# Optimization experiments

Measured on AMD Instinct MI355X. Metric: run time of the kernel, lower is better.

The kernel has to match this reference:

```python
import jax, jax.numpy as jnp
import numpy as np

B, T, C, H = 1, 4096, 3072, 24
D = C // H  # 128


def _make_rope_freqs(t, d):
    # comfy-style rotation matrices: [t, d//2, 2, 2] with rows [[cos,-sin],[sin,cos]]
    half = d // 2
    inv = 1.0 / (10000.0 ** (np.arange(half, dtype=np.float64) / half))
    ang = np.arange(t, dtype=np.float64)[:, None] * inv[None, :]
    cos, sin = np.cos(ang), np.sin(ang)
    f = np.stack([np.stack([cos, -sin], -1), np.stack([sin, cos], -1)], -2)
    return jnp.asarray(f, jnp.float32)


def setup_inputs() -> dict:
    key = jax.random.key(0)
    ks = jax.random.split(key, 6)
    s = 0.02  # typical init scale
    x = jax.random.normal(ks[0], (B, T, C), jnp.float32)
    context = jax.random.normal(ks[1], (B, T, C), jnp.float32)
    Wq = jax.random.normal(ks[2], (C, C), jnp.float32) * s
    Wk = jax.random.normal(ks[3], (C, C), jnp.float32) * s
    Wv = jax.random.normal(ks[4], (C, C), jnp.float32) * s
    Wo = jax.random.normal(ks[5], (C, C), jnp.float32) * s
    freqs = _make_rope_freqs(T, D)  # [T, D//2, 2, 2]
    return {"x": x, "context": context, "freqs": freqs,
            "Wq": Wq, "Wk": Wk, "Wv": Wv, "Wo": Wo}


def _apply_rope(t, freqs):
    # t: [B, T, H, D]; freqs: [T, D//2, 2, 2]
    b, tt, h, d = t.shape
    tr = t.reshape(b, tt, h, d // 2, 1, 2)
    f = freqs[:, None]  # [T, 1, D//2, 2, 2] -> broadcast over B, H
    out = f[..., 0] * tr[..., 0] + f[..., 1] * tr[..., 1]  # [B,T,H,D//2,2]
    return out.reshape(b, tt, h, d)


def reference(x, context, freqs, Wq, Wk, Wv, Wo):
    # QKV projections (torch Linear: y = x @ W.T), kept in BTHD layout
    q = (x @ Wq.T).reshape(B, T, H, D)
    k = (context @ Wk.T).reshape(B, -1, H, D)
    v = (context @ Wv.T).reshape(B, -1, H, D)
    # RoPE on q and k
    q = _apply_rope(q, freqs)
    k = _apply_rope(k, freqs)
    # SDPA, non-causal, scale 1/sqrt(D) (jax expects BTNH layout)
    out = jax.nn.dot_product_attention(q, k, v)
    return out.reshape(B, T, C) @ Wo.T
```

## Files before the change

### kernel.cpp

```cpp
#include <hip/hip_runtime.h>
#include <hip/hip_bf16.h>

#define TT 4096
#define CC 3072
#define HH 24
#define DD 128

typedef __bf16 bf16;
typedef __attribute__((ext_vector_type(8))) __bf16 bf16x8;
typedef __attribute__((ext_vector_type(4))) __bf16 bf16x4;
typedef __attribute__((ext_vector_type(4))) float f32x4;
typedef __attribute__((ext_vector_type(16))) float f32x16;
typedef __attribute__((ext_vector_type(4))) unsigned uint32x4;

#define MFMA(a,b,c)   __builtin_amdgcn_mfma_f32_16x16x32_bf16((a),(b),(c),0,0,0)
#define MFMA32(a,b,c) __builtin_amdgcn_mfma_f32_32x32x16_bf16((a),(b),(c),0,0,0)

static __device__ __forceinline__ unsigned packbf(float a, float b) {
  unsigned short ua = __builtin_bit_cast(unsigned short, (__bf16)a);
  unsigned short ub = __builtin_bit_cast(unsigned short, (__bf16)b);
  return (unsigned)ua | ((unsigned)ub << 16);
}
static __device__ __forceinline__ void plswap(unsigned &x, unsigned &y) {
  asm volatile("v_permlane32_swap_b32 %0, %1" : "+v"(x), "+v"(y));
}

template<int ABF, int OBF>
__global__ __launch_bounds__(256, 2)
void gemm_nt(const void* __restrict__ Ap, const float* __restrict__ Bp,
             void* __restrict__ Cp, int M, int N, int K) {
  __shared__ bf16 As[2][128][40];
  __shared__ bf16 Bs[2][128][40];
  const int tid = threadIdx.x;
  const int lane = tid & 63, wid = tid >> 6;
  const int m0 = blockIdx.y * 128, n0 = blockIdx.x * 128;
  const int wr = (wid >> 1) * 64, wc = (wid & 1) * 64;
  const int r = lane & 15, g = lane >> 4;
  const float* Af = (const float*)Ap;
  const bf16*  Ab = (const bf16*)Ap;

  f32x4 acc[4][4] = {};
  f32x4 pa[4], pb[4];
  bf16x8 qa[2];

  const int NT = K >> 5;

  auto load_tiles = [&](int kt) {
    const int kk = kt * 32;
    if constexpr (ABF) {
      #pragma unroll
      for (int j = 0; j < 2; ++j) {
        int c = tid + 256*j, row = c >> 2, kc = c & 3;
        qa[j] = *(const bf16x8*)(Ab + (size_t)(m0+row)*K + kk + kc*8);
      }
    } else {
      #pragma unroll
      for (int j = 0; j < 4; ++j) {
        int c = tid + 256*j, row = c >> 3, kc = c & 7;
        pa[j] = *(const f32x4*)(Af + (size_t)(m0+row)*K + kk + kc*4);
      }
    }
    #pragma unroll
    for (int j = 0; j < 4; ++j) {
      int c = tid + 256*j, row = c >> 3, kc = c & 7;
      pb[j] = *(const f32x4*)(Bp + (size_t)(n0+row)*K + kk + kc*4);
    }
  };

  auto write_tiles = [&](int buf) {
    if constexpr (ABF) {
      #pragma unroll
      for (int j = 0; j < 2; ++j) {
        int c = tid + 256*j, row = c >> 2, kc = c & 3;
        *(bf16x8*)&As[buf][row][kc*8] = qa[j];
      }
    } else {
      #pragma unroll
      for (int j = 0; j < 4; ++j) {
        int c = tid + 256*j, row = c >> 3, kc = c & 7;
        bf16x4 b;
        b[0]=(bf16)pa[j][0]; b[1]=(bf16)pa[j][1]; b[2]=(bf16)pa[j][2]; b[3]=(bf16)pa[j][3];
        *(bf16x4*)&As[buf][row][kc*4] = b;
      }
    }
    #pragma unroll
    for (int j = 0; j < 4; ++j) {
      int c = tid + 256*j, row = c >> 3, kc = c & 7;
      bf16x4 b;
      b[0]=(bf16)pb[j][0]; b[1]=(bf16)pb[j][1]; b[2]=(bf16)pb[j][2]; b[3]=(bf16)pb[j][3];
      *(bf16x4*)&Bs[buf][row][kc*4] = b;
    }
  };

  load_tiles(0);
  write_tiles(0);
  __syncthreads();

  for (int kt = 0; kt < NT; ++kt) {
    const int cur = kt & 1;
    if (kt + 1 < NT) load_tiles(kt + 1);
    bf16x8 af[4], bfr[4];
    #pragma unroll
    for (int m = 0; m < 4; ++m) af[m]  = *(const bf16x8*)&As[cur][wr + m*16 + r][g*8];
    #pragma unroll
    for (int n = 0; n < 4; ++n) bfr[n] = *(const bf16x8*)&Bs[cur][wc + n*16 + r][g*8];
    #pragma unroll
    for (int m = 0; m < 4; ++m)
      #pragma unroll
      for (int n = 0; n < 4; ++n)
        acc[m][n] = MFMA(af[m], bfr[n], acc[m][n]);
    if (kt + 1 < NT) write_tiles((kt + 1) & 1);
    __syncthreads();
  }

  #pragma unroll
  for (int m = 0; m < 4; ++m)
    #pragma unroll
    for (int n = 0; n < 4; ++n) {
      const int col = n0 + wc + n*16 + r;
      #pragma unroll
      for (int j = 0; j < 4; ++j) {
        const int row = m0 + wr + m*16 + g*4 + j;
        float v = acc[m][n][j];
        if constexpr (OBF) ((bf16*)Cp)[(size_t)row*N + col] = (bf16)v;
        else               ((float*)Cp)[(size_t)row*N + col] = v;
      }
    }
}

__global__ __launch_bounds__(256)
void rope_kernel(bf16* __restrict__ X, const float* __restrict__ F, float scale) {
  const int i = blockIdx.x * 256 + threadIdx.x;
  const size_t e8 = (size_t)i * 8;
  const int t  = (int)(e8 / CC);
  const int c  = (int)(e8 % CC);
  const int hc = c & (DD - 1);
  const float4* f = (const float4*)(F + (size_t)t*256 + (hc>>1)*4);
  bf16x8 v = *(const bf16x8*)(X + e8);
  bf16x8 o;
  #pragma unroll
  for (int p = 0; p < 4; ++p) {
    float x0 = (float)v[2*p], x1 = (float)v[2*p+1];
    float4 ff = f[p];
    o[2*p]   = (bf16)((ff.x*x0 + ff.y*x1) * scale);
    o[2*p+1] = (bf16)((ff.z*x0 + ff.w*x1) * scale);
  }
  *(bf16x8*)(X + e8) = o;
}

__global__ __launch_bounds__(256)
void transpose_v(const bf16* __restrict__ V, bf16* __restrict__ Vt) {
  __shared__ bf16 tile[64 * 128];
  const int t0 = blockIdx.x * 64, h = blockIdx.y;
  const int tid = threadIdx.x;
  #pragma unroll
  for (int j = 0; j < 4; ++j) {
    int c = tid + 256*j, t = c >> 4, c16 = c & 15;
    uint4 val = *(const uint4*)(V + (size_t)(t0+t)*CC + h*DD + c16*8);
    int sw = ((t & 7) ^ ((t >> 3) & 7)) << 4;
    *(uint4*)((char*)tile + t*256 + ((c16*16) ^ sw)) = val;
  }
  __syncthreads();
  #pragma unroll
  for (int j = 0; j < 4; ++j) {
    int c = tid + 256*j, d = c >> 3, c8 = c & 7;
    bf16x8 o;
    #pragma unroll
    for (int i = 0; i < 8; ++i) {
      int t = c8*8 + i;
      int sw = ((t & 7) ^ ((t >> 3) & 7)) << 4;
      o[i] = *(const bf16*)((char*)tile + t*256 + ((d*2) ^ sw));
    }
    *(bf16x8*)(Vt + (size_t)(h*DD + d)*TT + t0 + c8*8) = o;
  }
}

__global__ __launch_bounds__(256, 3)
void attn_kernel(const bf16* __restrict__ Q, const bf16* __restrict__ Kb,
                 const bf16* __restrict__ Vt, bf16* __restrict__ O) {
  __shared__ bf16 Ks[64 * 128];
  __shared__ bf16 Vs[128 * 64];

  const int tid = threadIdx.x, lane = tid & 63, wid = tid >> 6;
  const int c31 = lane & 31, g2 = lane >> 5;

  const int bid = blockIdx.x;
  const int fid = (bid & 7) * 96 + (bid >> 3);
  const int h = fid >> 5, qt = fid & 31;
  const int qrow = qt * 128 + wid * 32 + c31;

  bf16x8 aq[8];
  {
    const bf16* qp = Q + (size_t)qrow * CC + h * DD + g2 * 8;
    #pragma unroll
    for (int d0 = 0; d0 < 8; ++d0) aq[d0] = *(const bf16x8*)(qp + d0 * 16);
  }

  float m_ = -1e30f, l_ = 0.f;
  f32x16 o_[4] = {};

  auto stage = [&](int kv0) {
    uint4 kr[4], vr4[4];
    #pragma unroll
    for (int j = 0; j < 4; ++j) {
      int cc = tid + 256*j, row = cc >> 4, c16 = cc & 15;
      kr[j] = *(const uint4*)(Kb + (size_t)(kv0 + row) * CC + h * DD + c16 * 8);
    }
    #pragma unroll
    for (int j = 0; j < 4; ++j) {
      int cc = tid + 256*j, row = cc >> 3, c8 = cc & 7;
      vr4[j] = *(const uint4*)(Vt + (size_t)(h * DD + row) * TT + kv0 + c8 * 8);
    }
    #pragma unroll
    for (int j = 0; j < 4; ++j) {
      int cc = tid + 256*j, row = cc >> 4, c16 = cc & 15;
      *(uint4*)((char*)Ks + row * 256 + ((c16 * 16) ^ ((row & 7) << 4))) = kr[j];
    }
    #pragma unroll
    for (int j = 0; j < 4; ++j) {
      int cc = tid + 256*j, row = cc >> 3, c8 = cc & 7;
      *(uint4*)((char*)Vs + row * 128 + ((c8 * 16) ^ ((row & 7) << 4))) = vr4[j];
    }
  };

  const int NT = TT / 64;
  for (int t = 0; t < NT; ++t) {
    if (t) __syncthreads();
    stage(t * 64);
    __syncthreads();

    f32x16 s[2] = {};
    __builtin_amdgcn_s_setprio(1);
    #pragma unroll
    for (int d0 = 0; d0 < 8; ++d0) {
      #pragma unroll
      for (int tt = 0; tt < 2; ++tt) {
        const int kvr = tt * 32 + c31;
        bf16x8 ak = *(const bf16x8*)((const char*)Ks + kvr * 256 +
                                     ((d0 * 32 + g2 * 16) ^ ((kvr & 7) << 4)));
        s[tt] = MFMA32(ak, aq[d0], s[tt]);
      }
    }
    __builtin_amdgcn_s_setprio(0);

    float mx = s[0][0];
    #pragma unroll
    for (int i = 1; i < 16; ++i) mx = fmaxf(mx, s[0][i]);
    #pragma unroll
    for (int i = 0; i < 16; ++i) mx = fmaxf(mx, s[1][i]);
    mx = fmaxf(mx, __shfl_xor(mx, 32, 64));
    if (!__all(mx <= m_ + 8.f)) {
      float mn = fmaxf(m_, mx);
      float al = __expf(m_ - mn);
      l_ *= al;
      #pragma unroll
      for (int d0 = 0; d0 < 4; ++d0) o_[d0] *= al;
      m_ = mn;
    }

    unsigned w0[8], w1[8];
    float rs = 0.f;
    #pragma unroll
    for (int jj = 0; jj < 8; ++jj) {
      float a0 = __expf(s[0][2*jj] - m_), b0 = __expf(s[0][2*jj+1] - m_);
      float a1 = __expf(s[1][2*jj] - m_), b1 = __expf(s[1][2*jj+1] - m_);
      rs += (a0 + b0) + (a1 + b1);
      w0[jj] = packbf(a0, b0);
      w1[jj] = packbf(a1, b1);
    }
    rs += __shfl_xor(rs, 32, 64);
    l_ += rs;

    bf16x8 pb[4];
    #pragma unroll
    for (int t2 = 0; t2 < 4; ++t2) {
      const int jA = (t2 & 1) * 4;
      unsigned x0, y0, x1, y1;
      if (t2 < 2) { x0 = w0[jA]; y0 = w0[jA+2]; x1 = w0[jA+1]; y1 = w0[jA+3]; }
      else        { x0 = w1[jA]; y0 = w1[jA+2]; x1 = w1[jA+1]; y1 = w1[jA+3]; }
      plswap(x0, y0);
      plswap(x1, y1);
      uint32x4 uu; uu[0] = x0; uu[1] = x1; uu[2] = y0; uu[3] = y1;
      pb[t2] = __builtin_bit_cast(bf16x8, uu);
    }

    __builtin_amdgcn_s_setprio(1);
    #pragma unroll
    for (int d0 = 0; d0 < 4; ++d0) {
      const int vr = d0 * 32 + c31;
      #pragma unroll
      for (int t2 = 0; t2 < 4; ++t2) {
        bf16x8 av = *(const bf16x8*)((const char*)Vs + vr * 128 +
                                     ((t2 * 32 + g2 * 16) ^ ((vr & 7) << 4)));
        o_[d0] = MFMA32(av, pb[t2], o_[d0]);
      }
    }
    __builtin_amdgcn_s_setprio(0);
  }

  const float inv = 1.f / l_;
  bf16* orow = O + (size_t)qrow * CC + h * DD;
  #pragma unroll
  for (int d0 = 0; d0 < 4; ++d0)
    #pragma unroll
    for (int q4 = 0; q4 < 4; ++q4) {
      uint2 val;
      val.x = packbf(o_[d0][q4*4 + 0] * inv, o_[d0][q4*4 + 1] * inv);
      val.y = packbf(o_[d0][q4*4 + 2] * inv, o_[d0][q4*4 + 3] * inv);
      *(uint2*)(orow + d0*32 + q4*8 + g2*4) = val;
    }
}

extern "C" void kernel_launch(void* const* d_in, const int* in_sizes, int n_in,
                              void* d_out, int out_size, void* d_ws, size_t ws_size,
                              hipStream_t stream) {
  const float* x   = (const float*)d_in[0];
  const float* ctx = (const float*)d_in[1];
  const float* fr  = (const float*)d_in[2];
  const float* Wq  = (const float*)d_in[3];
  const float* Wk  = (const float*)d_in[4];
  const float* Wv  = (const float*)d_in[5];
  const float* Wo  = (const float*)d_in[6];
  float* out = (float*)d_out;
  char* ws = (char*)d_ws;

  const size_t SZ = (size_t)TT * CC * sizeof(bf16);
  bf16* Qb  = (bf16*)(ws);
  bf16* Kbf = (bf16*)(ws + SZ);
  bf16* Vb  = (bf16*)(ws + 2*SZ);
  bf16* Vtb = (bf16*)(ws + 3*SZ);
  bf16* Ob  = Vb;

  dim3 gg(CC/128, TT/128);
  gemm_nt<0,1><<<gg, 256, 0, stream>>>(x,   Wq, Qb,  TT, CC, CC);
  gemm_nt<0,1><<<gg, 256, 0, stream>>>(ctx, Wk, Kbf, TT, CC, CC);
  gemm_nt<0,1><<<gg, 256, 0, stream>>>(ctx, Wv, Vb,  TT, CC, CC);

  const int rblocks = (TT*CC/8)/256;
  rope_kernel<<<rblocks, 256, 0, stream>>>(Qb,  fr, 0.08838834764831845f);
  rope_kernel<<<rblocks, 256, 0, stream>>>(Kbf, fr, 1.0f);

  transpose_v<<<dim3(TT/64, HH), 256, 0, stream>>>(Vb, Vtb);
  attn_kernel<<<dim3(768), 256, 0, stream>>>(Qb, Kbf, Vtb, Ob);

  gemm_nt<1,0><<<gg, 256, 0, stream>>>(Ob, Wo, out, TT, CC, CC);
}
```

Before: 836.0 us.

## Fold log2e into Q scale, use exp2, packed bf16 convert and max3 in attention

The attention softmax now uses the native exp2 instruction: the Q pre-scale is multiplied by log2(e), so exponentials skip the extra multiply that __expf needs. Row-max reduction switches to v_max3_f32, and bf16 packing uses the hardware v_cvt_pk_bf16_f32 instead of two scalar converts plus shifts. Launch bounds for attention rise from 3 to 4 blocks per SIMD-group target, which may force register spilling. The changes trim VALU work in the softmax inner loop of an MFMA-bound kernel, and the attention kernel is only part of the total pipeline time.

```diff
diff --git a/kernel.cpp b/kernel.cpp
--- a/kernel.cpp
+++ b/kernel.cpp
@@ -16,10 +16,15 @@
 #define MFMA(a,b,c)   __builtin_amdgcn_mfma_f32_16x16x32_bf16((a),(b),(c),0,0,0)
 #define MFMA32(a,b,c) __builtin_amdgcn_mfma_f32_32x32x16_bf16((a),(b),(c),0,0,0)
 
-static __device__ __forceinline__ unsigned packbf(float a, float b) {
-  unsigned short ua = __builtin_bit_cast(unsigned short, (__bf16)a);
-  unsigned short ub = __builtin_bit_cast(unsigned short, (__bf16)b);
-  return (unsigned)ua | ((unsigned)ub << 16);
+static __device__ __forceinline__ unsigned cvtpk(float lo, float hi) {
+  unsigned r;
+  asm("v_cvt_pk_bf16_f32 %0, %1, %2" : "=v"(r) : "v"(lo), "v"(hi));
+  return r;
+}
+static __device__ __forceinline__ float max3f(float a, float b, float c) {
+  float r;
+  asm("v_max3_f32 %0, %1, %2, %3" : "=v"(r) : "v"(a), "v"(b), "v"(c));
+  return r;
 }
 static __device__ __forceinline__ void plswap(unsigned &x, unsigned &y) {
   asm volatile("v_permlane32_swap_b32 %0, %1" : "+v"(x), "+v"(y));
@@ -175,7 +180,7 @@
   }
 }
 
-__global__ __launch_bounds__(256, 3)
+__global__ __launch_bounds__(256, 4)
 void attn_kernel(const bf16* __restrict__ Q, const bf16* __restrict__ Kb,
                  const bf16* __restrict__ Vt, bf16* __restrict__ O) {
   __shared__ bf16 Ks[64 * 128];
@@ -243,15 +248,15 @@
     }
     __builtin_amdgcn_s_setprio(0);
 
-    float mx = s[0][0];
-    #pragma unroll
-    for (int i = 1; i < 16; ++i) mx = fmaxf(mx, s[0][i]);
-    #pragma unroll
-    for (int i = 0; i < 16; ++i) mx = fmaxf(mx, s[1][i]);
+    float mx = fmaxf(s[0][0], s[0][1]);
+    #pragma unroll
+    for (int i = 2; i < 16; i += 2) mx = max3f(mx, s[0][i], s[0][i+1]);
+    #pragma unroll
+    for (int i = 0; i < 16; i += 2) mx = max3f(mx, s[1][i], s[1][i+1]);
     mx = fmaxf(mx, __shfl_xor(mx, 32, 64));
     if (!__all(mx <= m_ + 8.f)) {
       float mn = fmaxf(m_, mx);
-      float al = __expf(m_ - mn);
+      float al = __builtin_amdgcn_exp2f(m_ - mn);
       l_ *= al;
       #pragma unroll
       for (int d0 = 0; d0 < 4; ++d0) o_[d0] *= al;
@@ -262,11 +267,13 @@
     float rs = 0.f;
     #pragma unroll
     for (int jj = 0; jj < 8; ++jj) {
-      float a0 = __expf(s[0][2*jj] - m_), b0 = __expf(s[0][2*jj+1] - m_);
-      float a1 = __expf(s[1][2*jj] - m_), b1 = __expf(s[1][2*jj+1] - m_);
+      float a0 = __builtin_amdgcn_exp2f(s[0][2*jj] - m_);
+      float b0 = __builtin_amdgcn_exp2f(s[0][2*jj+1] - m_);
+      float a1 = __builtin_amdgcn_exp2f(s[1][2*jj] - m_);
+      float b1 = __builtin_amdgcn_exp2f(s[1][2*jj+1] - m_);
       rs += (a0 + b0) + (a1 + b1);
-      w0[jj] = packbf(a0, b0);
-      w1[jj] = packbf(a1, b1);
+      w0[jj] = cvtpk(a0, b0);
+      w1[jj] = cvtpk(a1, b1);
     }
     rs += __shfl_xor(rs, 32, 64);
     l_ += rs;
@@ -305,8 +312,8 @@
     #pragma unroll
     for (int q4 = 0; q4 < 4; ++q4) {
       uint2 val;
-      val.x = packbf(o_[d0][q4*4 + 0] * inv, o_[d0][q4*4 + 1] * inv);
-      val.y = packbf(o_[d0][q4*4 + 2] * inv, o_[d0][q4*4 + 3] * inv);
+      val.x = cvtpk(o_[d0][q4*4 + 0] * inv, o_[d0][q4*4 + 1] * inv);
+      val.y = cvtpk(o_[d0][q4*4 + 2] * inv, o_[d0][q4*4 + 3] * inv);
       *(uint2*)(orow + d0*32 + q4*8 + g2*4) = val;
     }
 }
@@ -337,7 +344,7 @@
   gemm_nt<0,1><<<gg, 256, 0, stream>>>(ctx, Wv, Vb,  TT, CC, CC);
 
   const int rblocks = (TT*CC/8)/256;
-  rope_kernel<<<rblocks, 256, 0, stream>>>(Qb,  fr, 0.08838834764831845f);
+  rope_kernel<<<rblocks, 256, 0, stream>>>(Qb,  fr, 0.12751743314942355f);
   rope_kernel<<<rblocks, 256, 0, stream>>>(Kbf, fr, 1.0f);
 
   transpose_v<<<dim3(TT/64, HH), 256, 0, stream>>>(Vb, Vtb);
```

Result: slower. 1.062 ms (+27.1%).
